# Kernel optimization log

Hardware: AMD Instinct MI355X
Metric: run time of the kernel (lower is better)

## Reference

```python
import jax, jax.numpy as jnp
import numpy as np

N_CLASS, N_SUPPORT, N_QUERY = 5, 5, 15
C, T, V = 128, 8, 25
LN_EPS = 1e-12


def setup_inputs() -> dict:
    key = jax.random.key(0)
    ks = jax.random.split(key, 6)
    n_tot = N_CLASS * (N_SUPPORT + N_QUERY)
    inp = jax.random.normal(ks[0], (n_tot, C, T, V), dtype=jnp.float32)
    # episode labels: 20 consecutive samples per class (arange // per_class)
    target = (jnp.arange(n_tot, dtype=jnp.int32) // (N_SUPPORT + N_QUERY)).astype(jnp.int32)
    s = 0.02
    p = lambda k: jax.random.normal(k, (C, C), dtype=jnp.float32) * s
    return {
        'input': inp,
        'Wq': p(ks[1]), 'bq': jnp.zeros((C,), jnp.float32),
        'Wk': p(ks[2]), 'bk': jnp.zeros((C,), jnp.float32),
        'Wv': p(ks[3]), 'bv': jnp.zeros((C,), jnp.float32),
        'Wo': p(ks[4]), 'bo': jnp.zeros((C,), jnp.float32),
        'ln_g': jnp.ones((C,), jnp.float32), 'ln_b': jnp.zeros((C,), jnp.float32),
        'target': target,
        'n_support': N_SUPPORT,
    }


def _layer_norm(x, g, b):
    mu = x.mean(-1, keepdims=True)
    var = ((x - mu) ** 2).mean(-1, keepdims=True)
    return (x - mu) * jax.lax.rsqrt(var + LN_EPS) * g + b


def _episode_forward(input, Wq, bq, Wk, bk, Wv, bv, Wo, bo, ln_g, ln_b, target, n_support):
    n_tot, c, t, v = input.shape
    m = N_CLASS
    per_class = n_tot // m
    n_query = per_class - n_support
    n = m * n_query

    # support/query split (stable argsort == torch.where per class for sorted labels)
    order = jnp.argsort(target).reshape(m, per_class)
    supp_idx = order[:, :n_support]                      # (m, h)
    qry_idx = order[:, n_support:].reshape(-1)           # (n,)
    z_proto = input[supp_idx]                            # (m, h, c, t, v)
    zq = input[qry_idx]                                  # (n, c, t, v)

    # ---- hal(): pairwise cross-attention over the vertex axis ----
    mh = m * n_support
    zq_p = jnp.transpose(zq, (0, 2, 3, 1))                                   # (n, t, v, c)
    zp_p = jnp.transpose(z_proto.reshape(mh, c, t, v), (0, 2, 3, 1))          # (mh, t, v, c)
    cat = jnp.concatenate([zq_p, zp_p], axis=0)                               # (n1, t, v, c)
    n1 = cat.shape[0]

    # Q from each of the n1 items, K/V from each of the mh prototypes.
    # Equivalent to the original expand->reshape pairing, without duplicating K/V.
    Q = cat @ Wq + bq                                                         # (n1, t, v, c)
    K = zp_p @ Wk + bk                                                        # (mh, t, v, c)
    Vv = zp_p @ Wv + bv                                                       # (mh, t, v, c)
    scale = 1.0 / jnp.sqrt(jnp.asarray(c, dtype=Q.dtype))
    scores = jnp.einsum('ntqc,mtkc->nmtqk', Q, K) * scale                     # (n1, mh, t, v, v)
    attn = jax.nn.softmax(scores, axis=-1)
    ctx = jnp.einsum('nmtqk,mtkc->nmtqc', attn, Vv)                           # (n1, mh, t, v, c)
    out = _layer_norm(ctx @ Wo + bo + cat[:, None], ln_g, ln_b)               # residual + LN
    att = out.mean(axis=1)                                                    # (n1, t, v, c) mean over mh pairs

    zq_att = jnp.transpose(att[:n], (0, 3, 1, 2))                             # (n, c, t, v)
    proto_att = att[n:].reshape(m, n_support, t, v, c).mean(axis=1)           # (m, t, v, c)
    proto_att = jnp.transpose(proto_att, (0, 3, 1, 2))                        # (m, c, t, v)

    # ---- squared-Euclidean metric on flattened features ----
    zq_f = zq_att.reshape(n, -1)
    zp_f = proto_att.reshape(m, -1)
    dist = jnp.sum((zq_f[:, None, :] - zp_f[None, :, :]) ** 2, axis=-1)       # (n, m)

    log_p_y = jax.nn.log_softmax(-dist, axis=1).reshape(m, n_query, m)
    cls = jnp.arange(m)
    loss = -log_p_y[cls[:, None], jnp.arange(n_query)[None, :], cls[:, None]].mean()
    y_hat = jnp.argmax(log_p_y, axis=2)
    acc = (y_hat == cls[:, None]).astype(jnp.float32).mean()
    return loss, acc


def reference(input, Wq, bq, Wk, bk, Wv, bv, Wo, bo, ln_g, ln_b, target, n_support):
    return _episode_forward(input, Wq, bq, Wk, bk, Wv, bv, Wo, bo, ln_g, ln_b, target, n_support)
```

## Files before the change

kernel.cpp:

```cpp
#include <hip/hip_runtime.h>
#include <math.h>

#define NTOT 100
#define NQ   75
#define NP   25
#define CC   128
#define TT   8
#define VV   25
#define NCLS 5
#define NSUP 5
#define NQRY 15
#define ROW  (TT*VV*CC)
#define TILE (VV*CC)
#define ROWS_Q 20000
#define ROWS_S 5000
#define RB_Q 625
#define RB_S 157

typedef __attribute__((ext_vector_type(8))) short short8;
typedef __attribute__((ext_vector_type(16))) float f32x16;

typedef union { uint4 u4; short8 s8; } pk_t;

__device__ __forceinline__ ushort f2bf(float f) {
    uint u = __float_as_uint(f);
    u += 0x7FFFu + ((u >> 16) & 1u);
    return (ushort)(u >> 16);
}
__device__ __forceinline__ float bf2f(uint u16v) {
    return __uint_as_float(u16v << 16);
}
__device__ __forceinline__ uint pkbf(float a, float b) {
    return (uint)f2bf(a) | ((uint)f2bf(b) << 16);
}

__global__ __launch_bounds__(256) void k_proj(
    const float* __restrict__ input, const int* __restrict__ target,
    const float* __restrict__ Wq, const float* __restrict__ Wk,
    const float* __restrict__ Wv, const float* __restrict__ Wo,
    const float* __restrict__ bq, const float* __restrict__ bk,
    const float* __restrict__ bv,
    ushort* __restrict__ catC, ushort* __restrict__ Qf,
    ushort* __restrict__ Kf, ushort* __restrict__ Vf,
    int* __restrict__ counter) {
    __shared__ ushort stage[32 * 132];
    __shared__ ushort Wf[16384];
    __shared__ ushort VtF[4096];
    __shared__ int iscr[200];

    int bid = blockIdx.x, tid = threadIdx.x;
    int w = tid >> 6, lane = tid & 63, half = lane >> 5, l31 = lane & 31;

    if (bid == 0 && tid == 0) *counter = 0;

    if (tid < NTOT) iscr[tid] = target[tid];
    __syncthreads();
    if (tid < NTOT) {
        int ti = iscr[tid], rank = 0;
        for (int j = 0; j < NTOT; ++j) {
            int tj = iscr[j];
            rank += (tj < ti) || (tj == ti && j < tid);
        }
        iscr[100 + rank] = tid;
    }
    __syncthreads();

    bool isQ = bid >= RB_S;
    int rowblk = isQ ? bid - RB_S : bid;
    int rlimit = isQ ? ROWS_Q : ROWS_S;
    int g0 = rowblk * 32;
    int gend = min(g0 + 32, rlimit);

    for (int nn = g0 / 200; nn <= (gend - 1) / 200; ++nn) {
        int lo = max(g0 - nn * 200, 0);
        int hi = min(gend - 1 - nn * 200, 199);
        int len = hi - lo + 1;
        int nidx = isQ ? nn : (NQ + nn);
        int src;
        if (nidx < NQ) { int m = nidx / NQRY, qq = nidx - m * NQRY; src = iscr[100 + m * 20 + NSUP + qq]; }
        else           { int i2 = nidx - NQ; int m = i2 / NSUP, s = i2 - m * NSUP; src = iscr[100 + m * 20 + s]; }
        const float* inb = input + (size_t)src * ROW + lo;
        int rbase = nn * 200 + lo - g0;
        for (int idx = tid; idx < len * 128; idx += 256) {
            int c = idx / len, k = idx - c * len;
            stage[(rbase + k) * 132 + c] = f2bf(inb[c * 200 + k]);
        }
    }

    #define BUILDW(W) do {                                                       \
        for (int o = tid; o < 2048; o += 256) {                                  \
            int k8 = o >> 7, c = o & 127;                                        \
            uint4 pk;                                                            \
            pk.x = pkbf((W)[(k8*8+0)*128 + c], (W)[(k8*8+1)*128 + c]);           \
            pk.y = pkbf((W)[(k8*8+2)*128 + c], (W)[(k8*8+3)*128 + c]);           \
            pk.z = pkbf((W)[(k8*8+4)*128 + c], (W)[(k8*8+5)*128 + c]);           \
            pk.w = pkbf((W)[(k8*8+6)*128 + c], (W)[(k8*8+7)*128 + c]);           \
            int dst = (((c >> 5) * 8 + (k8 >> 1)) * 64 + ((c & 31) + 32 * (k8 & 1))) * 8; \
            *(uint4*)(Wf + dst) = pk;                                            \
        }                                                                        \
    } while (0)

    BUILDW(isQ ? Wq : Wk);
    __syncthreads();

    short8 af[8];
    #pragma unroll
    for (int ks = 0; ks < 8; ++ks)
        af[ks] = *(const short8*)&stage[l31 * 132 + ks * 16 + half * 8];

    #define CHAIN(A, OUT) do {                                                   \
        const ushort* bp_ = Wf + w * 4096 + lane * 8;                            \
        _Pragma("unroll")                                                        \
        for (int ks = 0; ks < 8; ++ks) {                                         \
            short8 bf_ = *(const short8*)(bp_ + ks * 512);                       \
            OUT = __builtin_amdgcn_mfma_f32_32x32x16_bf16(A[ks], bf_, OUT, 0, 0, 0); \
        }                                                                        \
    } while (0)

    if (isQ) {
        f32x16 Cm;
        #pragma unroll
        for (int r = 0; r < 16; ++r) Cm[r] = 0.f;
        CHAIN(af, Cm);
        float bcol = bq[w * 32 + l31];
        int c = w * 32 + l31;
        #pragma unroll
        for (int r = 0; r < 16; ++r) {
            int row = g0 + (r & 3) + 8 * (r >> 2) + 4 * half;
            int st = row / 25, vv = row - st * 25;
            size_t dst = (((size_t)st * 8 + (c >> 4)) * 64 + (vv + 32 * ((c >> 3) & 1))) * 8 + (c & 7);
            Qf[dst] = f2bf(Cm[r] + bcol);
        }
        uint* cc = (uint*)catC + (size_t)g0 * 64;
        for (int idx = tid; idx < 2048; idx += 256) {
            int row = idx >> 6, c2 = (idx & 63) * 2;
            cc[idx] = (uint)stage[row * 132 + c2] | ((uint)stage[row * 132 + c2 + 1] << 16);
        }
    } else {
        {
            f32x16 Cm;
            #pragma unroll
            for (int r = 0; r < 16; ++r) Cm[r] = 0.f;
            CHAIN(af, Cm);
            float bcol = bk[w * 32 + l31];
            int c = w * 32 + l31;
            #pragma unroll
            for (int r = 0; r < 16; ++r) {
                int row = g0 + (r & 3) + 8 * (r >> 2) + 4 * half;
                if (row < ROWS_S) {
                    int st = row / 25, vv = row - st * 25;
                    size_t dst = (((size_t)st * 8 + (c >> 4)) * 64 + (vv + 32 * ((c >> 3) & 1))) * 8 + (c & 7);
                    Kf[dst] = f2bf(Cm[r] + bcol);
                }
            }
        }
        __syncthreads();
        BUILDW(Wv);
        __syncthreads();
        {
            f32x16 Cm;
            #pragma unroll
            for (int r = 0; r < 16; ++r) Cm[r] = 0.f;
            CHAIN(af, Cm);
            float bcol = bv[w * 32 + l31];
            int c = w * 32 + l31;
            int ks2 = c >> 4, kh = (c >> 3) & 1, j2 = c & 7;
            #pragma unroll
            for (int r = 0; r < 16; ++r) {
                int rowLocal = (r & 3) + 8 * (r >> 2) + 4 * half;
                VtF[ks2 * 512 + (rowLocal + 32 * kh) * 8 + j2] = f2bf(Cm[r] + bcol);
            }
        }
        __syncthreads();
        BUILDW(Wo);
        __syncthreads();
        short8 a2[8];
        #pragma unroll
        for (int ks = 0; ks < 8; ++ks)
            a2[ks] = *(const short8*)&VtF[ks * 512 + lane * 8];
        {
            f32x16 Cm;
            #pragma unroll
            for (int r = 0; r < 16; ++r) Cm[r] = 0.f;
            CHAIN(a2, Cm);
            int c = w * 32 + l31;
            #pragma unroll
            for (int r = 0; r < 16; ++r) {
                int row = g0 + (r & 3) + 8 * (r >> 2) + 4 * half;
                if (row < ROWS_S) {
                    int tile = row / 25, vv = row - tile * 25;
                    size_t dst = ((((size_t)tile * 4 + (c >> 5)) * 2 + (vv >> 4)) * 64
                                  + ((c & 31) + 32 * ((vv & 15) >> 3))) * 8 + (vv & 7);
                    Vf[dst] = f2bf(Cm[r]);
                }
            }
        }
    }
    #undef CHAIN
    #undef BUILDW
}

__global__ __launch_bounds__(256, 2) void k_attn(
    const ushort* __restrict__ Qf, const ushort* __restrict__ Kf,
    const ushort* __restrict__ Vf, const ushort* __restrict__ catC,
    const float* __restrict__ bo, float* __restrict__ att) {
    __shared__ __align__(16) char smem[26016];
    float*  catb = (float*)smem;
    ushort* qls  = (ushort*)(smem + 12912);
    float (*red)[50][65] = (float (*)[50][65])smem;

    int pair = blockIdx.x;
    int t = pair & 7;
    int tid = threadIdx.x;
    int wv = tid >> 6, lane = tid & 63;
    int q = lane & 31, half = lane >> 5;

    {
        const uint* cc = (const uint*)catC + (size_t)pair * 1600;
        for (int i2 = tid; i2 < 1600; i2 += 256) {
            uint u = cc[i2];
            int r = i2 >> 6, c2 = (i2 & 63) * 2;
            catb[r * 129 + c2]     = bf2f(u & 0xffffu) + bo[c2];
            catb[r * 129 + c2 + 1] = bf2f(u >> 16) + bo[c2 + 1];
        }
    }
    {
        const uint* qp = (const uint*)(Qf + (size_t)pair * 4096);
        uint* ql = (uint*)qls;
        for (int i2 = tid; i2 < 2048; i2 += 256) ql[i2] = qp[i2];
    }
    __syncthreads();

    int qc = q < 25 ? q : 24;
    float attsum[64];
    #pragma unroll
    for (int i = 0; i < 64; ++i) attsum[i] = 0.f;
    float Csc = 0.f;

    const float CEXP = (float)(1.4426950408889634 * 0.08838834764831845);

    const ushort* kbase = Kf + (size_t)t * 4096 + lane * 8;
    short8 kf[8];
    #pragma unroll
    for (int ks = 0; ks < 8; ++ks)
        kf[ks] = *(const short8*)(kbase + (size_t)wv * 32768 + ks * 512);

    int cnt = (wv == 0) ? 7 : 6;
    for (int mi = 0; mi < cnt; ++mi) {
        int m = wv + 4 * mi;

        f32x16 S;
        #pragma unroll
        for (int r = 0; r < 16; ++r) S[r] = 0.f;
        #pragma unroll
        for (int ks = 0; ks < 8; ++ks) {
            short8 qv = *(const short8*)(qls + ks * 512 + lane * 8);
            S = __builtin_amdgcn_mfma_f32_32x32x16_bf16(kf[ks], qv, S, 0, 0, 0);
        }

        float p[16], mx = -3e38f;
        #pragma unroll
        for (int r = 0; r < 16; ++r) {
            int key = (r & 3) + 8 * (r >> 2) + 4 * half;
            float v = (key < 25) ? S[r] : -3e38f;
            p[r] = v; mx = fmaxf(mx, v);
        }
        mx = fmaxf(mx, __shfl_xor(mx, 32));
        float sum = 0.f;
        #pragma unroll
        for (int r = 0; r < 16; ++r) { p[r] = exp2f((p[r] - mx) * CEXP); sum += p[r]; }
        sum += __shfl_xor(sum, 32);
        float inv = 1.f / sum;

        const ushort* vp = Vf + ((size_t)(m * 8 + t)) * 4096 + lane * 8;
        short8 vf0 = *(const short8*)(vp);
        short8 vf1 = *(const short8*)(vp + 512);
        short8 vf2 = *(const short8*)(vp + 1024);
        short8 vf3 = *(const short8*)(vp + 1536);
        short8 vf4 = *(const short8*)(vp + 2048);
        short8 vf5 = *(const short8*)(vp + 2560);
        short8 vf6 = *(const short8*)(vp + 3072);
        short8 vf7 = *(const short8*)(vp + 3584);
        #pragma unroll
        for (int ks = 0; ks < 8; ++ks)
            kf[ks] = *(const short8*)(kbase + (size_t)(m + 4) * 32768 + ks * 512);

        uint o01   = pkbf(p[0] * inv,  p[1] * inv);
        uint o23   = pkbf(p[2] * inv,  p[3] * inv);
        uint o45   = pkbf(p[4] * inv,  p[5] * inv);
        uint o67   = pkbf(p[6] * inv,  p[7] * inv);
        uint o89   = pkbf(p[8] * inv,  p[9] * inv);
        uint o1011 = pkbf(p[10] * inv, p[11] * inv);
        uint o1213 = pkbf(p[12] * inv, p[13] * inv);
        uint o1415 = pkbf(p[14] * inv, p[15] * inv);
        bool h0 = (half == 0);
        uint rA = __shfl_xor(h0 ? o45 : o01, 32);
        uint rB = __shfl_xor(h0 ? o67 : o23, 32);
        uint rC = __shfl_xor(h0 ? o1213 : o89, 32);
        uint rD = __shfl_xor(h0 ? o1415 : o1011, 32);
        pk_t P0, P1;
        P0.u4 = h0 ? make_uint4(o01, o23, rA, rB) : make_uint4(rA, rB, o45, o67);
        P1.u4 = h0 ? make_uint4(o89, o1011, rC, rD) : make_uint4(rC, rD, o1213, o1415);
        short8 pb0 = P0.s8, pb1 = P1.s8;

        f32x16 ctx[4];
        #pragma unroll
        for (int mt = 0; mt < 4; ++mt) {
            #pragma unroll
            for (int r = 0; r < 16; ++r) ctx[mt][r] = 0.f;
        }
        ctx[0] = __builtin_amdgcn_mfma_f32_32x32x16_bf16(vf0, pb0, ctx[0], 0, 0, 0);
        ctx[0] = __builtin_amdgcn_mfma_f32_32x32x16_bf16(vf1, pb1, ctx[0], 0, 0, 0);
        ctx[1] = __builtin_amdgcn_mfma_f32_32x32x16_bf16(vf2, pb0, ctx[1], 0, 0, 0);
        ctx[1] = __builtin_amdgcn_mfma_f32_32x32x16_bf16(vf3, pb1, ctx[1], 0, 0, 0);
        ctx[2] = __builtin_amdgcn_mfma_f32_32x32x16_bf16(vf4, pb0, ctx[2], 0, 0, 0);
        ctx[2] = __builtin_amdgcn_mfma_f32_32x32x16_bf16(vf5, pb1, ctx[2], 0, 0, 0);
        ctx[3] = __builtin_amdgcn_mfma_f32_32x32x16_bf16(vf6, pb0, ctx[3], 0, 0, 0);
        ctx[3] = __builtin_amdgcn_mfma_f32_32x32x16_bf16(vf7, pb1, ctx[3], 0, 0, 0);

        float s1 = 0.f, s2 = 0.f;
        #pragma unroll
        for (int mt = 0; mt < 4; ++mt) {
            float t1 = 0.f, t2 = 0.f;
            #pragma unroll
            for (int r = 0; r < 16; ++r) {
                int c = mt * 32 + (r & 3) + 8 * (r >> 2) + 4 * half;
                float xv = ctx[mt][r] + catb[qc * 129 + c];
                ctx[mt][r] = xv;
                t1 += xv; t2 = fmaf(xv, xv, t2);
            }
            s1 += t1; s2 += t2;
        }
        s1 += __shfl_xor(s1, 32); s2 += __shfl_xor(s2, 32);
        float mu = s1 * (1.f / 128.f);
        float var = s2 * (1.f / 128.f) - mu * mu;
        var = fmaxf(var, 0.f);
        float rs = rsqrtf(var + 1e-12f);
        #pragma unroll
        for (int i = 0; i < 64; ++i)
            attsum[i] = fmaf(ctx[i >> 4][i & 15], rs, attsum[i]);
        Csc = fmaf(-mu, rs, Csc);
    }

    __syncthreads();
    int s = half * 25 + q;
    bool act = q < 25;
    if ((wv == 1 || wv == 3) && act) {
        float (*rg)[65] = red[wv >> 1];
        #pragma unroll
        for (int i = 0; i < 64; ++i) rg[s][i] = attsum[i];
        rg[s][64] = Csc;
    }
    __syncthreads();
    if ((wv == 0 || wv == 2) && act) {
        float (*rg)[65] = red[wv >> 1];
        #pragma unroll
        for (int i = 0; i < 64; ++i) attsum[i] += rg[s][i];
        Csc += rg[s][64];
    }
    __syncthreads();
    if (wv == 2 && act) {
        #pragma unroll
        for (int i = 0; i < 64; ++i) red[0][s][i] = attsum[i];
        red[0][s][64] = Csc;
    }
    __syncthreads();
    if (wv == 0 && act) {
        #pragma unroll
        for (int i = 0; i < 64; ++i) attsum[i] += red[0][s][i];
        Csc += red[0][s][64];
        float* ap = att + (size_t)pair * TILE + q * 128;
        #pragma unroll
        for (int mt = 0; mt < 4; ++mt) {
            #pragma unroll
            for (int rg4 = 0; rg4 < 4; ++rg4) {
                int c0 = mt * 32 + 8 * rg4 + 4 * half;
                int i0 = mt * 16 + rg4 * 4;
                float4 o;
                o.x = attsum[i0 + 0] + Csc; o.y = attsum[i0 + 1] + Csc;
                o.z = attsum[i0 + 2] + Csc; o.w = attsum[i0 + 3] + Csc;
                *(float4*)&ap[c0] = o;
            }
        }
    }
}

__global__ __launch_bounds__(256) void k_dist_loss(
    const float* __restrict__ att, const float* __restrict__ ln_g,
    float* __restrict__ dist, int* __restrict__ counter,
    float* __restrict__ out) {
    int b = blockIdx.x;
    int i = b / 5, j = b - 5 * i;
    const float4* a  = (const float4*)(att + (size_t)i * ROW);
    const float4* s0 = (const float4*)(att + (size_t)(NQ + j * 5 + 0) * ROW);
    const float4* s1p = (const float4*)(att + (size_t)(NQ + j * 5 + 1) * ROW);
    const float4* s2p = (const float4*)(att + (size_t)(NQ + j * 5 + 2) * ROW);
    const float4* s3p = (const float4*)(att + (size_t)(NQ + j * 5 + 3) * ROW);
    const float4* s4p = (const float4*)(att + (size_t)(NQ + j * 5 + 4) * ROW);
    float d = 0.f;
    for (int e4 = threadIdx.x; e4 < 6400; e4 += 256) {
        float4 av = a[e4];
        float4 q0 = s0[e4], q1 = s1p[e4], q2 = s2p[e4], q3 = s3p[e4], q4 = s4p[e4];
        float4 g4 = *(const float4*)(ln_g + (e4 & 31) * 4);
        float px = 0.2f * (q0.x + q1.x + q2.x + q3.x + q4.x);
        float py = 0.2f * (q0.y + q1.y + q2.y + q3.y + q4.y);
        float pz = 0.2f * (q0.z + q1.z + q2.z + q3.z + q4.z);
        float pw = 0.2f * (q0.w + q1.w + q2.w + q3.w + q4.w);
        float dx = av.x - px, dy = av.y - py, dz = av.z - pz, dw = av.w - pw;
        d = fmaf(g4.x * g4.x, dx * dx, d);
        d = fmaf(g4.y * g4.y, dy * dy, d);
        d = fmaf(g4.z * g4.z, dz * dz, d);
        d = fmaf(g4.w * g4.w, dw * dw, d);
    }
    #pragma unroll
    for (int msk = 32; msk >= 1; msk >>= 1) d += __shfl_xor(d, msk);
    __shared__ float part[4];
    __shared__ int lastFlag;
    int lane = threadIdx.x & 63, wv = threadIdx.x >> 6;
    if (lane == 0) part[wv] = d;
    __syncthreads();
    if (threadIdx.x == 0) {
        float total = (part[0] + part[1] + part[2] + part[3]) * (1.f / 625.f);
        __hip_atomic_store(&dist[b], total, __ATOMIC_RELEASE, __HIP_MEMORY_SCOPE_AGENT);
        int tk = __hip_atomic_fetch_add(counter, 1, __ATOMIC_ACQ_REL, __HIP_MEMORY_SCOPE_AGENT);
        lastFlag = (tk == 374);
    }
    __syncthreads();
    if (!lastFlag) return;

    int iq = threadIdx.x;
    float li = 0.f, ok = 0.f;
    if (iq < NQ) {
        float dd[5];
        #pragma unroll
        for (int jj = 0; jj < 5; ++jj)
            dd[jj] = __hip_atomic_load(&dist[iq * 5 + jj], __ATOMIC_ACQUIRE, __HIP_MEMORY_SCOPE_AGENT);
        int cls = iq / NQRY;
        float mind = dd[0];
        int best = 0;
        #pragma unroll
        for (int jj = 1; jj < 5; ++jj) {
            if (dd[jj] < mind) mind = dd[jj];
            if (dd[jj] < dd[best]) best = jj;
        }
        float sume = 0.f;
        #pragma unroll
        for (int jj = 0; jj < 5; ++jj) sume += expf(mind - dd[jj]);
        float lse = logf(sume) - mind;
        li = dd[cls] + lse;
        ok = (best == cls) ? 1.f : 0.f;
    }
    #pragma unroll
    for (int msk = 32; msk >= 1; msk >>= 1) {
        li += __shfl_xor(li, msk);
        ok += __shfl_xor(ok, msk);
    }
    if (lane == 0) { part[wv] = li; part[wv + 2] = ok; }
    __syncthreads();
    if (threadIdx.x == 0) {
        out[0] = (part[0] + part[1]) / 75.f;
        out[1] = (part[2] + part[3]) / 75.f;
    }
}

extern "C" void kernel_launch(void* const* d_in, const int* in_sizes, int n_in,
                              void* d_out, int out_size, void* d_ws, size_t ws_size,
                              hipStream_t stream) {
    const float* input = (const float*)d_in[0];
    const float* Wq   = (const float*)d_in[1];
    const float* bq   = (const float*)d_in[2];
    const float* Wk   = (const float*)d_in[3];
    const float* bk   = (const float*)d_in[4];
    const float* Wv   = (const float*)d_in[5];
    const float* bv   = (const float*)d_in[6];
    const float* Wo   = (const float*)d_in[7];
    const float* bo   = (const float*)d_in[8];
    const float* ln_g = (const float*)d_in[9];
    const float* ln_b = (const float*)d_in[10];
    const int* target = (const int*)d_in[11];
    float* out = (float*)d_out;
    (void)ln_b;

    float* ws = (float*)d_ws;
    ushort* catC = (ushort*)ws;
    ushort* Qf   = catC + 2560000;
    ushort* Kf   = Qf + 3276800;
    ushort* Vf   = Kf + 819200;
    float*  att  = (float*)(Vf + 819200);
    float*  distb = att + 2560000;
    int*    counter = (int*)(distb + 512);

    k_proj<<<RB_Q + RB_S, 256, 0, stream>>>(input, target, Wq, Wk, Wv, Wo, bq, bk, bv,
                                            catC, Qf, Kf, Vf, counter);
    k_attn<<<800, 256, 0, stream>>>(Qf, Kf, Vf, catC, bo, att);
    k_dist_loss<<<375, 256, 0, stream>>>(att, ln_g, distb, counter, out);
}
```

Baseline: 180.4 us.

## Prepack bf16 weights once globally and precompute prototype means before distance

A new small kernel converts the four 128x128 weight matrices to the bf16 MFMA-fragment layout once into global workspace. k_proj then reads B fragments straight from global memory instead of rebuilding them in shared memory in every block with extra barriers. A second new kernel averages the five support rows per class into a prototype buffer that reuses the catC region, so k_dist_loss reads two rows instead of six per block. Two launches are added and MFMA operands now come from global or L2 rather than LDS.

```diff
diff --git a/kernel.cpp b/kernel.cpp
--- a/kernel.cpp
+++ b/kernel.cpp
@@ -34,17 +34,34 @@
     return (uint)f2bf(a) | ((uint)f2bf(b) << 16);
 }
 
+__global__ __launch_bounds__(256) void k_pack(
+    const float* __restrict__ Wq, const float* __restrict__ Wk,
+    const float* __restrict__ Wv, const float* __restrict__ Wo,
+    ushort* __restrict__ WfG) {
+    int which = blockIdx.x;
+    const float* W = (which == 0) ? Wq : (which == 1) ? Wk : (which == 2) ? Wv : Wo;
+    ushort* dstbase = WfG + (size_t)which * 16384;
+    for (int o = threadIdx.x; o < 2048; o += 256) {
+        int k8 = o >> 7, c = o & 127;
+        uint4 pk;
+        pk.x = pkbf(W[(k8*8+0)*128 + c], W[(k8*8+1)*128 + c]);
+        pk.y = pkbf(W[(k8*8+2)*128 + c], W[(k8*8+3)*128 + c]);
+        pk.z = pkbf(W[(k8*8+4)*128 + c], W[(k8*8+5)*128 + c]);
+        pk.w = pkbf(W[(k8*8+6)*128 + c], W[(k8*8+7)*128 + c]);
+        int dst = (((c >> 5) * 8 + (k8 >> 1)) * 64 + ((c & 31) + 32 * (k8 & 1))) * 8;
+        *(uint4*)(dstbase + dst) = pk;
+    }
+}
+
 __global__ __launch_bounds__(256) void k_proj(
     const float* __restrict__ input, const int* __restrict__ target,
-    const float* __restrict__ Wq, const float* __restrict__ Wk,
-    const float* __restrict__ Wv, const float* __restrict__ Wo,
+    const ushort* __restrict__ WfG,
     const float* __restrict__ bq, const float* __restrict__ bk,
     const float* __restrict__ bv,
     ushort* __restrict__ catC, ushort* __restrict__ Qf,
     ushort* __restrict__ Kf, ushort* __restrict__ Vf,
     int* __restrict__ counter) {
     __shared__ ushort stage[32 * 132];
-    __shared__ ushort Wf[16384];
     __shared__ ushort VtF[4096];
     __shared__ int iscr[200];
 
@@ -86,21 +103,6 @@
             stage[(rbase + k) * 132 + c] = f2bf(inb[c * 200 + k]);
         }
     }
-
-    #define BUILDW(W) do {                                                       \
-        for (int o = tid; o < 2048; o += 256) {                                  \
-            int k8 = o >> 7, c = o & 127;                                        \
-            uint4 pk;                                                            \
-            pk.x = pkbf((W)[(k8*8+0)*128 + c], (W)[(k8*8+1)*128 + c]);           \
-            pk.y = pkbf((W)[(k8*8+2)*128 + c], (W)[(k8*8+3)*128 + c]);           \
-            pk.z = pkbf((W)[(k8*8+4)*128 + c], (W)[(k8*8+5)*128 + c]);           \
-            pk.w = pkbf((W)[(k8*8+6)*128 + c], (W)[(k8*8+7)*128 + c]);           \
-            int dst = (((c >> 5) * 8 + (k8 >> 1)) * 64 + ((c & 31) + 32 * (k8 & 1))) * 8; \
-            *(uint4*)(Wf + dst) = pk;                                            \
-        }                                                                        \
-    } while (0)
-
-    BUILDW(isQ ? Wq : Wk);
     __syncthreads();
 
     short8 af[8];
@@ -108,8 +110,8 @@
     for (int ks = 0; ks < 8; ++ks)
         af[ks] = *(const short8*)&stage[l31 * 132 + ks * 16 + half * 8];
 
-    #define CHAIN(A, OUT) do {                                                   \
-        const ushort* bp_ = Wf + w * 4096 + lane * 8;                            \
+    #define CHAIN(A, OUT, BASE) do {                                             \
+        const ushort* bp_ = (BASE) + w * 4096 + lane * 8;                        \
         _Pragma("unroll")                                                        \
         for (int ks = 0; ks < 8; ++ks) {                                         \
             short8 bf_ = *(const short8*)(bp_ + ks * 512);                       \
@@ -121,7 +123,7 @@
         f32x16 Cm;
         #pragma unroll
         for (int r = 0; r < 16; ++r) Cm[r] = 0.f;
-        CHAIN(af, Cm);
+        CHAIN(af, Cm, WfG);
         float bcol = bq[w * 32 + l31];
         int c = w * 32 + l31;
         #pragma unroll
@@ -141,7 +143,7 @@
             f32x16 Cm;
             #pragma unroll
             for (int r = 0; r < 16; ++r) Cm[r] = 0.f;
-            CHAIN(af, Cm);
+            CHAIN(af, Cm, WfG + 16384);
             float bcol = bk[w * 32 + l31];
             int c = w * 32 + l31;
             #pragma unroll
@@ -154,14 +156,11 @@
                 }
             }
         }
-        __syncthreads();
-        BUILDW(Wv);
-        __syncthreads();
         {
             f32x16 Cm;
             #pragma unroll
             for (int r = 0; r < 16; ++r) Cm[r] = 0.f;
-            CHAIN(af, Cm);
+            CHAIN(af, Cm, WfG + 32768);
             float bcol = bv[w * 32 + l31];
             int c = w * 32 + l31;
             int ks2 = c >> 4, kh = (c >> 3) & 1, j2 = c & 7;
@@ -172,8 +171,6 @@
             }
         }
         __syncthreads();
-        BUILDW(Wo);
-        __syncthreads();
         short8 a2[8];
         #pragma unroll
         for (int ks = 0; ks < 8; ++ks)
@@ -182,7 +179,7 @@
             f32x16 Cm;
             #pragma unroll
             for (int r = 0; r < 16; ++r) Cm[r] = 0.f;
-            CHAIN(a2, Cm);
+            CHAIN(a2, Cm, WfG + 49152);
             int c = w * 32 + l31;
             #pragma unroll
             for (int r = 0; r < 16; ++r) {
@@ -197,7 +194,6 @@
         }
     }
     #undef CHAIN
-    #undef BUILDW
 }
 
 __global__ __launch_bounds__(256, 2) void k_attn(
@@ -385,28 +381,43 @@
     }
 }
 
+__global__ __launch_bounds__(256) void k_proto(
+    const float* __restrict__ att, float* __restrict__ proto) {
+    int b = blockIdx.x;
+    int j = b >> 3, chunk = b & 7;
+    const float4* s0 = (const float4*)(att + (size_t)(NQ + j * 5 + 0) * ROW);
+    const float4* s1 = (const float4*)(att + (size_t)(NQ + j * 5 + 1) * ROW);
+    const float4* s2 = (const float4*)(att + (size_t)(NQ + j * 5 + 2) * ROW);
+    const float4* s3 = (const float4*)(att + (size_t)(NQ + j * 5 + 3) * ROW);
+    const float4* s4 = (const float4*)(att + (size_t)(NQ + j * 5 + 4) * ROW);
+    float4* pr = (float4*)(proto + (size_t)j * ROW);
+    int e0 = chunk * 800, e1 = e0 + 800;
+    for (int e4 = e0 + threadIdx.x; e4 < e1; e4 += 256) {
+        float4 q0 = s0[e4], q1 = s1[e4], q2 = s2[e4], q3 = s3[e4], q4 = s4[e4];
+        float4 o;
+        o.x = 0.2f * (q0.x + q1.x + q2.x + q3.x + q4.x);
+        o.y = 0.2f * (q0.y + q1.y + q2.y + q3.y + q4.y);
+        o.z = 0.2f * (q0.z + q1.z + q2.z + q3.z + q4.z);
+        o.w = 0.2f * (q0.w + q1.w + q2.w + q3.w + q4.w);
+        pr[e4] = o;
+    }
+}
+
 __global__ __launch_bounds__(256) void k_dist_loss(
-    const float* __restrict__ att, const float* __restrict__ ln_g,
+    const float* __restrict__ att, const float* __restrict__ proto,
+    const float* __restrict__ ln_g,
     float* __restrict__ dist, int* __restrict__ counter,
     float* __restrict__ out) {
     int b = blockIdx.x;
     int i = b / 5, j = b - 5 * i;
-    const float4* a  = (const float4*)(att + (size_t)i * ROW);
-    const float4* s0 = (const float4*)(att + (size_t)(NQ + j * 5 + 0) * ROW);
-    const float4* s1p = (const float4*)(att + (size_t)(NQ + j * 5 + 1) * ROW);
-    const float4* s2p = (const float4*)(att + (size_t)(NQ + j * 5 + 2) * ROW);
-    const float4* s3p = (const float4*)(att + (size_t)(NQ + j * 5 + 3) * ROW);
-    const float4* s4p = (const float4*)(att + (size_t)(NQ + j * 5 + 4) * ROW);
+    const float4* a = (const float4*)(att + (size_t)i * ROW);
+    const float4* p = (const float4*)(proto + (size_t)j * ROW);
     float d = 0.f;
     for (int e4 = threadIdx.x; e4 < 6400; e4 += 256) {
         float4 av = a[e4];
-        float4 q0 = s0[e4], q1 = s1p[e4], q2 = s2p[e4], q3 = s3p[e4], q4 = s4p[e4];
+        float4 pv = p[e4];
         float4 g4 = *(const float4*)(ln_g + (e4 & 31) * 4);
-        float px = 0.2f * (q0.x + q1.x + q2.x + q3.x + q4.x);
-        float py = 0.2f * (q0.y + q1.y + q2.y + q3.y + q4.y);
-        float pz = 0.2f * (q0.z + q1.z + q2.z + q3.z + q4.z);
-        float pw = 0.2f * (q0.w + q1.w + q2.w + q3.w + q4.w);
-        float dx = av.x - px, dy = av.y - py, dz = av.z - pz, dw = av.w - pw;
+        float dx = av.x - pv.x, dy = av.y - pv.y, dz = av.z - pv.z, dw = av.w - pv.w;
         d = fmaf(g4.x * g4.x, dx * dx, d);
         d = fmaf(g4.y * g4.y, dy * dy, d);
         d = fmaf(g4.z * g4.z, dz * dz, d);
@@ -489,9 +500,13 @@
     float*  att  = (float*)(Vf + 819200);
     float*  distb = att + 2560000;
     int*    counter = (int*)(distb + 512);
-
-    k_proj<<<RB_Q + RB_S, 256, 0, stream>>>(input, target, Wq, Wk, Wv, Wo, bq, bk, bv,
+    ushort* WfG  = (ushort*)(counter + 16);
+    float*  proto = (float*)catC;
+
+    k_pack<<<4, 256, 0, stream>>>(Wq, Wk, Wv, Wo, WfG);
+    k_proj<<<RB_Q + RB_S, 256, 0, stream>>>(input, target, WfG, bq, bk, bv,
                                             catC, Qf, Kf, Vf, counter);
     k_attn<<<800, 256, 0, stream>>>(Qf, Kf, Vf, catC, bo, att);
-    k_dist_loss<<<375, 256, 0, stream>>>(att, ln_g, distb, counter, out);
-}
+    k_proto<<<40, 256, 0, stream>>>(att, proto);
+    k_dist_loss<<<375, 256, 0, stream>>>(att, proto, ln_g, distb, counter, out);
+}
```

New measurement: 176.0 us. 2.4% less time.
